# Optimization experiments

Hardware: AMD Instinct MI355X
Metric: run time of the kernel (lower is better)

Reference implementation:

```python
import jax, jax.numpy as jnp
import numpy as np

N_HEAD = 16


def setup_inputs() -> dict:
    key = jax.random.key(0)
    ks = jax.random.split(key, 3)
    B, T, C = 4, 2048, 1024
    x = jax.random.normal(ks[0], (B, T, C), dtype=jnp.float32)
    w_attn = jax.random.normal(ks[1], (3 * C, C), dtype=jnp.float32) * (1.0 / np.sqrt(C))
    b_attn = jnp.zeros((3 * C,), dtype=jnp.float32)
    w_proj = jax.random.normal(ks[2], (C, C), dtype=jnp.float32) * (1.0 / np.sqrt(C))
    b_proj = jnp.zeros((C,), dtype=jnp.float32)
    return {"x": x, "w_attn": w_attn, "b_attn": b_attn, "w_proj": w_proj, "b_proj": b_proj}


def reference(x, w_attn, b_attn, w_proj, b_proj):
    B, T, C = x.shape
    H = N_HEAD
    D = C // H
    qkv = x @ w_attn.T + b_attn                      # [B, T, 3C]
    q, k, v = jnp.split(qkv, 3, axis=-1)
    # [B, T, C] -> [B, H, T, D]
    q = q.reshape(B, T, H, D).transpose(0, 2, 1, 3)
    k = k.reshape(B, T, H, D).transpose(0, 2, 1, 3)
    v = v.reshape(B, T, H, D).transpose(0, 2, 1, 3)
    scale = 1.0 / np.sqrt(D).astype(np.float32)
    att = jnp.einsum('bhqd,bhkd->bhqk', q, k) * scale  # [B, H, T, T]
    causal = jnp.tril(jnp.ones((T, T), dtype=bool))
    att = jnp.where(causal[None, None], att, -jnp.inf)
    att = jax.nn.softmax(att, axis=-1)
    y = jnp.einsum('bhqk,bhkd->bhqd', att, v)          # [B, H, T, D]
    y = y.transpose(0, 2, 1, 3).reshape(B, T, C)
    return y @ w_proj.T + b_proj
```

## Files before the change

kernel.cpp:

```cpp
#include <hip/hip_runtime.h>
#include <hip/hip_bf16.h>
#include <stdint.h>

typedef __attribute__((ext_vector_type(8))) short bf16x8;
typedef __attribute__((ext_vector_type(4))) float f32x4;

#define MFMA16(a, b, c) __builtin_amdgcn_mfma_f32_16x16x32_bf16((a), (b), (c), 0, 0, 0)

__device__ __forceinline__ unsigned short f2bf(float f) {
  unsigned int u = __builtin_bit_cast(unsigned int, f);
  unsigned int r = (u + 0x7fffu + ((u >> 16) & 1u)) >> 16;
  return (unsigned short)r;
}

__device__ __forceinline__ void gload16(const unsigned short* g, unsigned short* lds_dst) {
  __builtin_amdgcn_global_load_lds(
      (const __attribute__((address_space(1))) unsigned int*)g,
      (__attribute__((address_space(3))) unsigned int*)lds_dst, 16, 0, 0);
}

__global__ void cvt_f32_bf16(const float* __restrict__ in, unsigned short* __restrict__ out, long n) {
  long i = ((long)blockIdx.x * blockDim.x + threadIdx.x) * 4;
  long stride = (long)gridDim.x * blockDim.x * 4;
  for (; i < n; i += stride) {
    float4 v = *(const float4*)(in + i);
    ushort4 o;
    o.x = f2bf(v.x); o.y = f2bf(v.y); o.z = f2bf(v.z); o.w = f2bf(v.w);
    *(ushort4*)(out + i) = o;
  }
}

template <int EPI>
__global__ __launch_bounds__(256, 2)
void gemm_bt(const unsigned short* __restrict__ A,
             const unsigned short* __restrict__ Bt,
             const float* __restrict__ bias,
             int M, int N, int K,
             unsigned short* __restrict__ q_out,
             unsigned short* __restrict__ k_out,
             unsigned short* __restrict__ vt_out,
             float* __restrict__ f_out) {
  alignas(16) __shared__ unsigned short Abuf[128 * 32];
  alignas(16) __shared__ unsigned short Bbuf[128 * 32];
  const int t = threadIdx.x, w = t >> 6, l = t & 63;
  const int bm = blockIdx.x, bn = blockIdx.y;
  const int wm = w >> 1, wn = w & 1;
  const int lo = l & 15, hi = l >> 4;

  f32x4 acc[4][4];
  const f32x4 zero = {0.f, 0.f, 0.f, 0.f};
#pragma unroll
  for (int i = 0; i < 4; ++i)
#pragma unroll
    for (int j = 0; j < 4; ++j) acc[i][j] = zero;

  const int srow = w * 32 + (l >> 2);
  const int scol = (l & 3) * 8;
  const long arow0 = (long)bm * 128;
  const long brow0 = (long)bn * 128;
  unsigned short* Asub = Abuf + w * 1024;
  unsigned short* Bsub = Bbuf + w * 1024;

  for (int k0 = 0; k0 < K; k0 += 32) {
    __syncthreads();
    gload16(A + (arow0 + srow) * K + k0 + scol, Asub);
    gload16(A + (arow0 + srow + 16) * K + k0 + scol, Asub + 512);
    gload16(Bt + (brow0 + srow) * K + k0 + scol, Bsub);
    gload16(Bt + (brow0 + srow + 16) * K + k0 + scol, Bsub + 512);
    __syncthreads();
    bf16x8 af[4], bfr[4];
#pragma unroll
    for (int i = 0; i < 4; ++i)
      af[i] = *(const bf16x8*)&Abuf[(wm * 64 + i * 16 + lo) * 32 + hi * 8];
#pragma unroll
    for (int j = 0; j < 4; ++j)
      bfr[j] = *(const bf16x8*)&Bbuf[(wn * 64 + j * 16 + lo) * 32 + hi * 8];
#pragma unroll
    for (int i = 0; i < 4; ++i)
#pragma unroll
      for (int j = 0; j < 4; ++j)
        acc[i][j] = MFMA16(af[i], bfr[j], acc[i][j]);
  }

#pragma unroll
  for (int i = 0; i < 4; ++i) {
#pragma unroll
    for (int j = 0; j < 4; ++j) {
#pragma unroll
      for (int r = 0; r < 4; ++r) {
        int row = bm * 128 + wm * 64 + i * 16 + hi * 4 + r;
        int col = bn * 128 + wn * 64 + j * 16 + lo;
        float v = acc[i][j][r] + bias[col];
        if (EPI == 0) {
          int b = row >> 11, tt = row & 2047;
          int seg = col >> 10, cc = col & 1023;
          int h = cc >> 6, d = cc & 63;
          long bh = (long)(b * 16 + h);
          if (seg == 0)      q_out[(bh * 2048 + tt) * 64 + d] = f2bf(v * 0.1803368801111f);
          else if (seg == 1) k_out[(bh * 2048 + tt) * 64 + d] = f2bf(v);
          else               vt_out[(bh * 64 + d) * 2048 + tt] = f2bf(v);
        } else {
          f_out[(long)row * N + col] = v;
        }
      }
    }
  }
}

__global__ __launch_bounds__(512, 4)
void attn_kernel(const unsigned short* __restrict__ Q,
                 const unsigned short* __restrict__ K,
                 const unsigned short* __restrict__ Vt,
                 unsigned short* __restrict__ Y) {
  alignas(16) __shared__ unsigned short Kbuf[2][64 * 64];
  alignas(16) __shared__ unsigned short Vbuf[2][64 * 64];
  alignas(16) __shared__ unsigned short pbuf[8][16 * 64];
  const int t = threadIdx.x, w = t >> 6, l = t & 63;
  const int lo = l & 15, hi = l >> 4;
  const int bh = blockIdx.x;
  const int p = blockIdx.y;
  const int b = bh >> 4, h = bh & 15;
  const int sA = p, sB = 15 - p;
  const int nA = 2 * p + 2;
  const int nTot = 34;
  const unsigned short* Qp = Q + (long)bh * 2048 * 64;
  const unsigned short* Kp = K + (long)bh * 2048 * 64;
  const unsigned short* Vp = Vt + (long)bh * 64 * 2048;
  unsigned short* pw = pbuf[w];

  const short one_bf = (short)0x3F80;
  const bf16x8 ones = {one_bf, one_bf, one_bf, one_bf, one_bf, one_bf, one_bf, one_bf};
  const f32x4 zero = {0.f, 0.f, 0.f, 0.f};

  const int qbA = sA * 128 + w * 16;
  const int qbB = sB * 128 + w * 16;

  bf16x8 qf0, qf1;
  float mcol;
  f32x4 lsum;
  f32x4 oacc[4];

  qf0 = *(const bf16x8*)&Qp[(qbA + lo) * 64 + hi * 8];
  qf1 = *(const bf16x8*)&Qp[(qbA + lo) * 64 + 32 + hi * 8];
  mcol = -__builtin_inff();
  lsum = zero;
#pragma unroll
  for (int dg = 0; dg < 4; ++dg) oacc[dg] = zero;

  const int srow = t >> 3;
  const int scw = ((t & 7) ^ (srow & 7)) * 8;
  const int sw = lo & 7;

#define STAGE(kvoff, bufidx)                                          \
  do {                                                                \
    unsigned short* KB_ = Kbuf[bufidx] + w * 512;                     \
    unsigned short* VB_ = Vbuf[bufidx] + w * 512;                     \
    gload16(Kp + (long)((kvoff) + srow) * 64 + scw, KB_);             \
    gload16(Vp + (long)srow * 2048 + (kvoff) + scw, VB_);             \
  } while (0)

  STAGE(0, 0);
  __syncthreads();

  for (int g = 0; g < nTot; ++g) {
    const bool inA = (g < nA);
    const int kvb = (inA ? g : g - nA) * 64;
    const int cur = g & 1;
    if (g + 1 < nTot) {
      const int jn = (g + 1 < nA) ? g + 1 : g + 1 - nA;
      STAGE(jn * 64, cur ^ 1);
    }
    const int qbase = inA ? qbA : qbB;
    if (kvb <= qbase + 15) {
      const unsigned short* KB = Kbuf[cur];
      const unsigned short* VB = Vbuf[cur];
      f32x4 s[4];
#pragma unroll
      for (int cg = 0; cg < 4; ++cg) s[cg] = zero;
      __builtin_amdgcn_s_setprio(1);
#pragma unroll
      for (int cg = 0; cg < 4; ++cg) {
        bf16x8 k0 = *(const bf16x8*)&KB[(cg * 16 + lo) * 64 + ((hi) ^ sw) * 8];
        bf16x8 k1 = *(const bf16x8*)&KB[(cg * 16 + lo) * 64 + ((4 + hi) ^ sw) * 8];
        s[cg] = MFMA16(k0, qf0, s[cg]);
        s[cg] = MFMA16(k1, qf1, s[cg]);
      }
      __builtin_amdgcn_s_setprio(0);
      if (kvb + 63 > qbase) {
        const int limit = qbase + lo - kvb;
#pragma unroll
        for (int cg = 0; cg < 4; ++cg)
#pragma unroll
          for (int r = 0; r < 4; ++r)
            if (cg * 16 + hi * 4 + r > limit) s[cg][r] = -__builtin_inff();
      }
      float pm = fmaxf(fmaxf(fmaxf(s[0][0], s[0][1]), fmaxf(s[0][2], s[0][3])),
                       fmaxf(fmaxf(s[1][0], s[1][1]), fmaxf(s[1][2], s[1][3])));
      pm = fmaxf(pm, fmaxf(fmaxf(fmaxf(s[2][0], s[2][1]), fmaxf(s[2][2], s[2][3])),
                           fmaxf(fmaxf(s[3][0], s[3][1]), fmaxf(s[3][2], s[3][3]))));
      pm = fmaxf(pm, __shfl_xor(pm, 16));
      pm = fmaxf(pm, __shfl_xor(pm, 32));
      float mn;
      if (__all(pm <= mcol + 11.54f)) {
        mn = mcol;
      } else {
        mn = fmaxf(mcol, pm);
        float a = exp2f(mcol - mn);
        mcol = mn;
        float ar[4];
#pragma unroll
        for (int r = 0; r < 4; ++r) ar[r] = __shfl(a, hi * 4 + r);
#pragma unroll
        for (int r = 0; r < 4; ++r) {
          lsum[r] *= ar[r];
#pragma unroll
          for (int dg = 0; dg < 4; ++dg) oacc[dg][r] *= ar[r];
        }
      }
#pragma unroll
      for (int cg = 0; cg < 4; ++cg) {
        float p0 = exp2f(s[cg][0] - mn);
        float p1 = exp2f(s[cg][1] - mn);
        float p2 = exp2f(s[cg][2] - mn);
        float p3 = exp2f(s[cg][3] - mn);
        unsigned int u0, u1;
        asm("v_cvt_pk_bf16_f32 %0, %1, %2" : "=v"(u0) : "v"(p0), "v"(p1));
        asm("v_cvt_pk_bf16_f32 %0, %1, %2" : "=v"(u1) : "v"(p2), "v"(p3));
        const int gg = (cg * 2 + (hi >> 1)) ^ sw;
        uint2 val; val.x = u0; val.y = u1;
        *(uint2*)&pw[lo * 64 + gg * 8 + (hi & 1) * 4] = val;
      }
      asm volatile("s_waitcnt lgkmcnt(0)" ::: "memory");
      bf16x8 pa0 = *(const bf16x8*)&pw[lo * 64 + ((hi) ^ sw) * 8];
      bf16x8 pa1 = *(const bf16x8*)&pw[lo * 64 + ((4 + hi) ^ sw) * 8];
      __builtin_amdgcn_s_setprio(1);
      lsum = MFMA16(pa0, ones, lsum);
      lsum = MFMA16(pa1, ones, lsum);
#pragma unroll
      for (int dg = 0; dg < 4; ++dg) {
        bf16x8 vv0 = *(const bf16x8*)&VB[(dg * 16 + lo) * 64 + ((hi) ^ sw) * 8];
        bf16x8 vv1 = *(const bf16x8*)&VB[(dg * 16 + lo) * 64 + ((4 + hi) ^ sw) * 8];
        oacc[dg] = MFMA16(pa0, vv0, oacc[dg]);
        oacc[dg] = MFMA16(pa1, vv1, oacc[dg]);
      }
      __builtin_amdgcn_s_setprio(0);
    }
    if (g == nA - 1) {
#pragma unroll
      for (int r = 0; r < 4; ++r) {
        float inv = 1.0f / lsum[r];
        int rowg = qbA + hi * 4 + r;
        long base = ((long)b * 2048 + rowg) * 1024 + h * 64;
#pragma unroll
        for (int dg = 0; dg < 4; ++dg)
          Y[base + dg * 16 + lo] = f2bf(oacc[dg][r] * inv);
      }
      qf0 = *(const bf16x8*)&Qp[(qbB + lo) * 64 + hi * 8];
      qf1 = *(const bf16x8*)&Qp[(qbB + lo) * 64 + 32 + hi * 8];
      mcol = -__builtin_inff();
      lsum = zero;
#pragma unroll
      for (int dg = 0; dg < 4; ++dg) oacc[dg] = zero;
    }
    __syncthreads();
  }

#pragma unroll
  for (int r = 0; r < 4; ++r) {
    float inv = 1.0f / lsum[r];
    int rowg = qbB + hi * 4 + r;
    long base = ((long)b * 2048 + rowg) * 1024 + h * 64;
#pragma unroll
    for (int dg = 0; dg < 4; ++dg)
      Y[base + dg * 16 + lo] = f2bf(oacc[dg][r] * inv);
  }
#undef STAGE
}

extern "C" void kernel_launch(void* const* d_in, const int* in_sizes, int n_in,
                              void* d_out, int out_size, void* d_ws, size_t ws_size,
                              hipStream_t stream) {
  const float* x      = (const float*)d_in[0];
  const float* w_attn = (const float*)d_in[1];
  const float* b_attn = (const float*)d_in[2];
  const float* w_proj = (const float*)d_in[3];
  const float* b_proj = (const float*)d_in[4];
  float* out = (float*)d_out;

  const long NX = 8192L * 1024;
  const long NWA = 3072L * 1024;
  const long NWP = 1024L * 1024;
  const long NQ = 64L * 2048 * 64;

  char* ws = (char*)d_ws;
  unsigned short* xb  = (unsigned short*)ws; ws += NX * 2;
  unsigned short* wab = (unsigned short*)ws; ws += NWA * 2;
  unsigned short* wpb = (unsigned short*)ws; ws += NWP * 2;
  unsigned short* qb  = (unsigned short*)ws; ws += NQ * 2;
  unsigned short* kb  = (unsigned short*)ws; ws += NQ * 2;
  unsigned short* vtb = (unsigned short*)ws; ws += NQ * 2;
  unsigned short* yb  = (unsigned short*)ws; ws += NX * 2;

  cvt_f32_bf16<<<2048, 256, 0, stream>>>(x, xb, NX);
  cvt_f32_bf16<<<768, 256, 0, stream>>>(w_attn, wab, NWA);
  cvt_f32_bf16<<<256, 256, 0, stream>>>(w_proj, wpb, NWP);

  dim3 g1(64, 24);
  gemm_bt<0><<<g1, 256, 0, stream>>>(xb, wab, b_attn, 8192, 3072, 1024,
                                     qb, kb, vtb, nullptr);
  dim3 ga(64, 8);
  attn_kernel<<<ga, 512, 0, stream>>>(qb, kb, vtb, yb);
  dim3 g2(64, 8);
  gemm_bt<1><<<g2, 256, 0, stream>>>(yb, wpb, b_proj, 8192, 1024, 1024,
                                     nullptr, nullptr, nullptr, out);
}
```

Before: 198.2 us.

## Rewrite GEMM main loop with 3-stage LDS pipeline, swizzle, and 128x256 tiles

The QKV and output-projection GEMM now uses 512-thread blocks computing 128x256 tiles with K-step 64. A triple-buffered LDS ring is fed by direct global-to-LDS loads interleaved with MFMA phases, and the LDS layout is XOR-swizzled to avoid bank conflicts. The goal is to hide global-load latency and raise MFMA utilization compared with the single-buffered loop that synced twice per 32-wide K step. It hardcodes 16 K-iterations (K=1024) and raises LDS use to about 144KB per block, which limits occupancy.

```diff
diff --git a/kernel.cpp b/kernel.cpp
--- a/kernel.cpp
+++ b/kernel.cpp
@@ -31,7 +31,7 @@
 }
 
 template <int EPI>
-__global__ __launch_bounds__(256, 2)
+__global__ __launch_bounds__(512, 2)
 void gemm_bt(const unsigned short* __restrict__ A,
              const unsigned short* __restrict__ Bt,
              const float* __restrict__ bias,
@@ -40,12 +40,12 @@
              unsigned short* __restrict__ k_out,
              unsigned short* __restrict__ vt_out,
              float* __restrict__ f_out) {
-  alignas(16) __shared__ unsigned short Abuf[128 * 32];
-  alignas(16) __shared__ unsigned short Bbuf[128 * 32];
+  alignas(16) __shared__ unsigned short Ash[3][128 * 64];
+  alignas(16) __shared__ unsigned short Bsh[3][256 * 64];
   const int t = threadIdx.x, w = t >> 6, l = t & 63;
   const int bm = blockIdx.x, bn = blockIdx.y;
-  const int wm = w >> 1, wn = w & 1;
-  const int lo = l & 15, hi = l >> 4;
+  const int wm = w >> 2, wn = w & 3;
+  const int lo = l & 15, hi = l >> 4, swk = l & 7;
 
   f32x4 acc[4][4];
   const f32x4 zero = {0.f, 0.f, 0.f, 0.f};
@@ -54,33 +54,135 @@
 #pragma unroll
     for (int j = 0; j < 4; ++j) acc[i][j] = zero;
 
-  const int srow = w * 32 + (l >> 2);
-  const int scol = (l & 3) * 8;
-  const long arow0 = (long)bm * 128;
-  const long brow0 = (long)bn * 128;
-  unsigned short* Asub = Abuf + w * 1024;
-  unsigned short* Bsub = Bbuf + w * 1024;
-
-  for (int k0 = 0; k0 < K; k0 += 32) {
-    __syncthreads();
-    gload16(A + (arow0 + srow) * K + k0 + scol, Asub);
-    gload16(A + (arow0 + srow + 16) * K + k0 + scol, Asub + 512);
-    gload16(Bt + (brow0 + srow) * K + k0 + scol, Bsub);
-    gload16(Bt + (brow0 + srow + 16) * K + k0 + scol, Bsub + 512);
-    __syncthreads();
-    bf16x8 af[4], bfr[4];
-#pragma unroll
-    for (int i = 0; i < 4; ++i)
-      af[i] = *(const bf16x8*)&Abuf[(wm * 64 + i * 16 + lo) * 32 + hi * 8];
-#pragma unroll
-    for (int j = 0; j < 4; ++j)
-      bfr[j] = *(const bf16x8*)&Bbuf[(wn * 64 + j * 16 + lo) * 32 + hi * 8];
-#pragma unroll
-    for (int i = 0; i < 4; ++i)
-#pragma unroll
-      for (int j = 0; j < 4; ++j)
-        acc[i][j] = MFMA16(af[i], bfr[j], acc[i][j]);
+  const int lr = l >> 3;
+  const int gsrc = ((l & 7) ^ lr) * 8;
+  const int rA0 = w * 16 + lr,     rA1 = w * 16 + 8 + lr;
+  const int rB0 = w * 32 + lr,     rB1 = w * 32 + 8 + lr;
+  const int rB2 = w * 32 + 16 + lr, rB3 = w * 32 + 24 + lr;
+  const unsigned short* sA0 = A + (long)(bm * 128 + rA0) * K + gsrc;
+  const unsigned short* sA1 = A + (long)(bm * 128 + rA1) * K + gsrc;
+  const unsigned short* sB0 = Bt + (long)(bn * 256 + rB0) * K + gsrc;
+  const unsigned short* sB1 = Bt + (long)(bn * 256 + rB1) * K + gsrc;
+  const unsigned short* sB2 = Bt + (long)(bn * 256 + rB2) * K + gsrc;
+  const unsigned short* sB3 = Bt + (long)(bn * 256 + rB3) * K + gsrc;
+
+#define STAGE_A(off, sb) do { unsigned short* d_ = &Ash[sb][w * 1024];        \
+    gload16(sA0 + (off), d_); gload16(sA1 + (off), d_ + 512); } while (0)
+#define STAGE_B01(off, sb) do { unsigned short* d_ = &Bsh[sb][w * 2048];      \
+    gload16(sB0 + (off), d_); gload16(sB1 + (off), d_ + 512); } while (0)
+#define STAGE_B23(off, sb) do { unsigned short* d_ = &Bsh[sb][w * 2048];      \
+    gload16(sB2 + (off), d_ + 1024); gload16(sB3 + (off), d_ + 1536); } while (0)
+
+  STAGE_A(0, 0);  STAGE_B01(0, 0);  STAGE_B23(0, 0);
+  STAGE_A(64, 1); STAGE_B01(64, 1); STAGE_B23(64, 1);
+  asm volatile("s_waitcnt vmcnt(6)" ::: "memory");
+  __builtin_amdgcn_sched_barrier(0);
+  __builtin_amdgcn_s_barrier();
+
+  const int ra = wm * 64 + lo;
+  const int rb = wn * 64 + lo;
+  const int g0 = (hi ^ swk) * 8;
+  const int g1 = ((4 + hi) ^ swk) * 8;
+
+  int cb = 0;
+  int koff = 128;
+  for (int kt = 0; kt < 16; ++kt) {
+    const unsigned short* As = Ash[cb];
+    const unsigned short* Bs = Bsh[cb];
+    int sb = cb + 2; if (sb >= 3) sb -= 3;
+    const bool st = (kt < 14);
+
+    bf16x8 a00 = *(const bf16x8*)&As[(ra)*64 + g0];
+    bf16x8 a01 = *(const bf16x8*)&As[(ra)*64 + g1];
+    bf16x8 a10 = *(const bf16x8*)&As[(ra + 16) * 64 + g0];
+    bf16x8 a11 = *(const bf16x8*)&As[(ra + 16) * 64 + g1];
+    bf16x8 b00 = *(const bf16x8*)&Bs[(rb)*64 + g0];
+    bf16x8 b01 = *(const bf16x8*)&Bs[(rb)*64 + g1];
+    bf16x8 b10 = *(const bf16x8*)&Bs[(rb + 16) * 64 + g0];
+    bf16x8 b11 = *(const bf16x8*)&Bs[(rb + 16) * 64 + g1];
+    if (st) STAGE_A(koff, sb);
+    __builtin_amdgcn_s_barrier();
+    asm volatile("s_waitcnt lgkmcnt(0)" ::: "memory");
+    __builtin_amdgcn_sched_barrier(0);
+    __builtin_amdgcn_s_setprio(1);
+    acc[0][0] = MFMA16(a00, b00, acc[0][0]);
+    acc[0][1] = MFMA16(a00, b10, acc[0][1]);
+    acc[1][0] = MFMA16(a10, b00, acc[1][0]);
+    acc[1][1] = MFMA16(a10, b10, acc[1][1]);
+    acc[0][0] = MFMA16(a01, b01, acc[0][0]);
+    acc[0][1] = MFMA16(a01, b11, acc[0][1]);
+    acc[1][0] = MFMA16(a11, b01, acc[1][0]);
+    acc[1][1] = MFMA16(a11, b11, acc[1][1]);
+    __builtin_amdgcn_s_setprio(0);
+    __builtin_amdgcn_sched_barrier(0);
+    __builtin_amdgcn_s_barrier();
+
+    bf16x8 b20 = *(const bf16x8*)&Bs[(rb + 32) * 64 + g0];
+    bf16x8 b21 = *(const bf16x8*)&Bs[(rb + 32) * 64 + g1];
+    bf16x8 b30 = *(const bf16x8*)&Bs[(rb + 48) * 64 + g0];
+    bf16x8 b31 = *(const bf16x8*)&Bs[(rb + 48) * 64 + g1];
+    if (st) STAGE_B01(koff, sb);
+    __builtin_amdgcn_s_barrier();
+    asm volatile("s_waitcnt lgkmcnt(0)" ::: "memory");
+    __builtin_amdgcn_sched_barrier(0);
+    __builtin_amdgcn_s_setprio(1);
+    acc[0][2] = MFMA16(a00, b20, acc[0][2]);
+    acc[0][3] = MFMA16(a00, b30, acc[0][3]);
+    acc[1][2] = MFMA16(a10, b20, acc[1][2]);
+    acc[1][3] = MFMA16(a10, b30, acc[1][3]);
+    acc[0][2] = MFMA16(a01, b21, acc[0][2]);
+    acc[0][3] = MFMA16(a01, b31, acc[0][3]);
+    acc[1][2] = MFMA16(a11, b21, acc[1][2]);
+    acc[1][3] = MFMA16(a11, b31, acc[1][3]);
+    __builtin_amdgcn_s_setprio(0);
+    __builtin_amdgcn_sched_barrier(0);
+    __builtin_amdgcn_s_barrier();
+
+    bf16x8 a20 = *(const bf16x8*)&As[(ra + 32) * 64 + g0];
+    bf16x8 a21 = *(const bf16x8*)&As[(ra + 32) * 64 + g1];
+    bf16x8 a30 = *(const bf16x8*)&As[(ra + 48) * 64 + g0];
+    bf16x8 a31 = *(const bf16x8*)&As[(ra + 48) * 64 + g1];
+    if (st) STAGE_B23(koff, sb);
+    __builtin_amdgcn_s_barrier();
+    asm volatile("s_waitcnt lgkmcnt(0)" ::: "memory");
+    __builtin_amdgcn_sched_barrier(0);
+    __builtin_amdgcn_s_setprio(1);
+    acc[2][2] = MFMA16(a20, b20, acc[2][2]);
+    acc[2][3] = MFMA16(a20, b30, acc[2][3]);
+    acc[3][2] = MFMA16(a30, b20, acc[3][2]);
+    acc[3][3] = MFMA16(a30, b30, acc[3][3]);
+    acc[2][2] = MFMA16(a21, b21, acc[2][2]);
+    acc[2][3] = MFMA16(a21, b31, acc[2][3]);
+    acc[3][2] = MFMA16(a31, b21, acc[3][2]);
+    acc[3][3] = MFMA16(a31, b31, acc[3][3]);
+    __builtin_amdgcn_s_setprio(0);
+    __builtin_amdgcn_sched_barrier(0);
+    __builtin_amdgcn_s_barrier();
+
+    __builtin_amdgcn_s_setprio(1);
+    acc[2][0] = MFMA16(a20, b00, acc[2][0]);
+    acc[2][1] = MFMA16(a20, b10, acc[2][1]);
+    acc[3][0] = MFMA16(a30, b00, acc[3][0]);
+    acc[3][1] = MFMA16(a30, b10, acc[3][1]);
+    acc[2][0] = MFMA16(a21, b01, acc[2][0]);
+    acc[2][1] = MFMA16(a21, b11, acc[2][1]);
+    acc[3][0] = MFMA16(a31, b01, acc[3][0]);
+    acc[3][1] = MFMA16(a31, b11, acc[3][1]);
+    __builtin_amdgcn_s_setprio(0);
+    if (kt < 14) {
+      asm volatile("s_waitcnt vmcnt(6)" ::: "memory");
+    } else if (kt == 14) {
+      asm volatile("s_waitcnt vmcnt(0)" ::: "memory");
+    }
+    __builtin_amdgcn_sched_barrier(0);
+    __builtin_amdgcn_s_barrier();
+
+    cb += 1; if (cb == 3) cb = 0;
+    koff += 64;
   }
+#undef STAGE_A
+#undef STAGE_B01
+#undef STAGE_B23
 
 #pragma unroll
   for (int i = 0; i < 4; ++i) {
@@ -89,7 +191,7 @@
 #pragma unroll
       for (int r = 0; r < 4; ++r) {
         int row = bm * 128 + wm * 64 + i * 16 + hi * 4 + r;
-        int col = bn * 128 + wn * 64 + j * 16 + lo;
+        int col = bn * 256 + wn * 64 + j * 16 + lo;
         float v = acc[i][j][r] + bias[col];
         if (EPI == 0) {
           int b = row >> 11, tt = row & 2047;
@@ -305,12 +407,12 @@
   cvt_f32_bf16<<<768, 256, 0, stream>>>(w_attn, wab, NWA);
   cvt_f32_bf16<<<256, 256, 0, stream>>>(w_proj, wpb, NWP);
 
-  dim3 g1(64, 24);
-  gemm_bt<0><<<g1, 256, 0, stream>>>(xb, wab, b_attn, 8192, 3072, 1024,
+  dim3 g1(64, 12);
+  gemm_bt<0><<<g1, 512, 0, stream>>>(xb, wab, b_attn, 8192, 3072, 1024,
                                      qb, kb, vtb, nullptr);
   dim3 ga(64, 8);
   attn_kernel<<<ga, 512, 0, stream>>>(qb, kb, vtb, yb);
-  dim3 g2(64, 8);
-  gemm_bt<1><<<g2, 256, 0, stream>>>(yb, wpb, b_proj, 8192, 1024, 1024,
+  dim3 g2(64, 4);
+  gemm_bt<1><<<g2, 512, 0, stream>>>(yb, wpb, b_proj, 8192, 1024, 1024,
                                      nullptr, nullptr, nullptr, out);
 }
```

New measurement: 195.3 us. About the same (-1.4%).

## Rewrite GEMM as 256x256 tile, 8-wave, double-buffered pipelined kernel with swizzled LDS

Applied to the files above, without the earlier changes.

The GEMM kernel moves from a 128x128 tile with 4 waves and single-buffered K=32 steps to a 256x256 tile with 8 waves. It uses K=64 steps with double-buffered LDS split into halves, an XOR swizzle on the LDS column layout, and an interleaved schedule. That schedule issues the next tile's global-to-LDS loads between MFMA quadrants, using explicit waitcnt, barriers and setprio. The aim is to hide global-load latency behind MFMA work, cut bank conflicts, and raise data reuse per block. The cost is larger register (acc[8][4]) and LDS footprint, fewer blocks (grid shrinks to 32x12 and 32x4), and a hardcoded K loop count of 16 that assumes K=1024.

```diff
diff --git a/kernel.cpp b/kernel.cpp
--- a/kernel.cpp
+++ b/kernel.cpp
@@ -31,7 +31,7 @@
 }
 
 template <int EPI>
-__global__ __launch_bounds__(256, 2)
+__global__ __launch_bounds__(512, 2)
 void gemm_bt(const unsigned short* __restrict__ A,
              const unsigned short* __restrict__ Bt,
              const float* __restrict__ bias,
@@ -40,56 +40,156 @@
              unsigned short* __restrict__ k_out,
              unsigned short* __restrict__ vt_out,
              float* __restrict__ f_out) {
-  alignas(16) __shared__ unsigned short Abuf[128 * 32];
-  alignas(16) __shared__ unsigned short Bbuf[128 * 32];
+  alignas(16) __shared__ unsigned short Alds[2][2][128 * 64];
+  alignas(16) __shared__ unsigned short Blds[2][2][128 * 64];
   const int t = threadIdx.x, w = t >> 6, l = t & 63;
   const int bm = blockIdx.x, bn = blockIdx.y;
-  const int wm = w >> 1, wn = w & 1;
-  const int lo = l & 15, hi = l >> 4;
-
-  f32x4 acc[4][4];
+  const int wm = w >> 2, wn = w & 3;
+  const int lo = l & 15, hi = l >> 4, swk = lo & 7;
+
+  f32x4 acc[8][4];
   const f32x4 zero = {0.f, 0.f, 0.f, 0.f};
 #pragma unroll
-  for (int i = 0; i < 4; ++i)
+  for (int i = 0; i < 8; ++i)
 #pragma unroll
     for (int j = 0; j < 4; ++j) acc[i][j] = zero;
 
-  const int srow = w * 32 + (l >> 2);
-  const int scol = (l & 3) * 8;
-  const long arow0 = (long)bm * 128;
-  const long brow0 = (long)bn * 128;
-  unsigned short* Asub = Abuf + w * 1024;
-  unsigned short* Bsub = Bbuf + w * 1024;
-
-  for (int k0 = 0; k0 < K; k0 += 32) {
-    __syncthreads();
-    gload16(A + (arow0 + srow) * K + k0 + scol, Asub);
-    gload16(A + (arow0 + srow + 16) * K + k0 + scol, Asub + 512);
-    gload16(Bt + (brow0 + srow) * K + k0 + scol, Bsub);
-    gload16(Bt + (brow0 + srow + 16) * K + k0 + scol, Bsub + 512);
-    __syncthreads();
-    bf16x8 af[4], bfr[4];
-#pragma unroll
-    for (int i = 0; i < 4; ++i)
-      af[i] = *(const bf16x8*)&Abuf[(wm * 64 + i * 16 + lo) * 32 + hi * 8];
-#pragma unroll
-    for (int j = 0; j < 4; ++j)
-      bfr[j] = *(const bf16x8*)&Bbuf[(wn * 64 + j * 16 + lo) * 32 + hi * 8];
-#pragma unroll
-    for (int i = 0; i < 4; ++i)
-#pragma unroll
-      for (int j = 0; j < 4; ++j)
-        acc[i][j] = MFMA16(af[i], bfr[j], acc[i][j]);
+  const int sr = t >> 3;
+  const int gsrcE = ((t & 7) ^ (sr & 7)) * 8;
+  const unsigned short* Asrc = A + (long)(bm * 256 + sr) * K + gsrcE;
+  const unsigned short* Bsrc = Bt + (long)(bn * 256 + ((sr >> 5) << 6) + (sr & 31)) * K + gsrcE;
+
+#define STAGE_AH(sb, qh, koff) do {                                    \
+    unsigned short* d_ = &Alds[sb][qh][w * 512];                       \
+    const unsigned short* s_ = Asrc + (long)(qh) * 64 * K + (koff);    \
+    gload16(s_, d_); gload16(s_ + 128L * K, d_ + 4096); } while (0)
+#define STAGE_BH(sb, hh, koff) do {                                    \
+    unsigned short* d_ = &Blds[sb][hh][w * 512];                       \
+    const unsigned short* s_ = Bsrc + (long)(hh) * 32 * K + (koff);    \
+    gload16(s_, d_); gload16(s_ + 128L * K, d_ + 4096); } while (0)
+
+  STAGE_AH(0, 0, 0);
+  STAGE_BH(0, 0, 0);
+  STAGE_BH(0, 1, 0);
+  STAGE_AH(0, 1, 0);
+  asm volatile("s_waitcnt vmcnt(4)" ::: "memory");
+  __builtin_amdgcn_sched_barrier(0);
+  __builtin_amdgcn_s_barrier();
+
+  const int lrA = (wm * 64 + lo) * 64;
+  const int lrB = (wn * 32 + lo) * 64;
+  const int gk0 = ((hi) ^ swk) * 8;
+  const int gk1 = ((4 + hi) ^ swk) * 8;
+
+  bf16x8 af[4][2], blo[2][2], bhi[2][2];
+
+  for (int kt = 0; kt < 16; ++kt) {
+    const int c = kt & 1, nb = c ^ 1;
+    const bool st = (kt < 15);
+    const int koff = (kt + 1) * 64;
+    const unsigned short* A0 = Alds[c][0];
+    const unsigned short* A1 = Alds[c][1];
+    const unsigned short* B0 = Blds[c][0];
+    const unsigned short* B1 = Blds[c][1];
+
+#pragma unroll
+    for (int ii = 0; ii < 4; ++ii) {
+      af[ii][0] = *(const bf16x8*)&A0[lrA + ii * 1024 + gk0];
+      af[ii][1] = *(const bf16x8*)&A0[lrA + ii * 1024 + gk1];
+    }
+#pragma unroll
+    for (int jj = 0; jj < 2; ++jj) {
+      blo[jj][0] = *(const bf16x8*)&B0[lrB + jj * 1024 + gk0];
+      blo[jj][1] = *(const bf16x8*)&B0[lrB + jj * 1024 + gk1];
+    }
+    if (st) STAGE_AH(nb, 0, koff);
+    __builtin_amdgcn_s_barrier();
+    asm volatile("s_waitcnt lgkmcnt(0)" ::: "memory");
+    __builtin_amdgcn_sched_barrier(0);
+    __builtin_amdgcn_s_setprio(1);
+#pragma unroll
+    for (int ii = 0; ii < 4; ++ii)
+#pragma unroll
+      for (int jj = 0; jj < 2; ++jj) {
+        acc[ii][jj] = MFMA16(af[ii][0], blo[jj][0], acc[ii][jj]);
+        acc[ii][jj] = MFMA16(af[ii][1], blo[jj][1], acc[ii][jj]);
+      }
+    __builtin_amdgcn_s_setprio(0);
+    if (st) { asm volatile("s_waitcnt vmcnt(4)" ::: "memory"); }
+    else    { asm volatile("s_waitcnt vmcnt(2)" ::: "memory"); }
+    __builtin_amdgcn_sched_barrier(0);
+    __builtin_amdgcn_s_barrier();
+
+#pragma unroll
+    for (int jj = 0; jj < 2; ++jj) {
+      bhi[jj][0] = *(const bf16x8*)&B1[lrB + jj * 1024 + gk0];
+      bhi[jj][1] = *(const bf16x8*)&B1[lrB + jj * 1024 + gk1];
+    }
+    if (st) STAGE_BH(nb, 0, koff);
+    __builtin_amdgcn_s_barrier();
+    asm volatile("s_waitcnt lgkmcnt(0)" ::: "memory");
+    __builtin_amdgcn_sched_barrier(0);
+    __builtin_amdgcn_s_setprio(1);
+#pragma unroll
+    for (int ii = 0; ii < 4; ++ii)
+#pragma unroll
+      for (int jj = 0; jj < 2; ++jj) {
+        acc[ii][2 + jj] = MFMA16(af[ii][0], bhi[jj][0], acc[ii][2 + jj]);
+        acc[ii][2 + jj] = MFMA16(af[ii][1], bhi[jj][1], acc[ii][2 + jj]);
+      }
+    __builtin_amdgcn_s_setprio(0);
+    if (st) { asm volatile("s_waitcnt vmcnt(4)" ::: "memory"); }
+    else    { asm volatile("s_waitcnt vmcnt(0)" ::: "memory"); }
+    __builtin_amdgcn_sched_barrier(0);
+    __builtin_amdgcn_s_barrier();
+
+#pragma unroll
+    for (int ii = 0; ii < 4; ++ii) {
+      af[ii][0] = *(const bf16x8*)&A1[lrA + ii * 1024 + gk0];
+      af[ii][1] = *(const bf16x8*)&A1[lrA + ii * 1024 + gk1];
+    }
+    if (st) STAGE_BH(nb, 1, koff);
+    __builtin_amdgcn_s_barrier();
+    asm volatile("s_waitcnt lgkmcnt(0)" ::: "memory");
+    __builtin_amdgcn_sched_barrier(0);
+    __builtin_amdgcn_s_setprio(1);
+#pragma unroll
+    for (int ii = 0; ii < 4; ++ii)
+#pragma unroll
+      for (int jj = 0; jj < 2; ++jj) {
+        acc[4 + ii][2 + jj] = MFMA16(af[ii][0], bhi[jj][0], acc[4 + ii][2 + jj]);
+        acc[4 + ii][2 + jj] = MFMA16(af[ii][1], bhi[jj][1], acc[4 + ii][2 + jj]);
+      }
+    __builtin_amdgcn_s_setprio(0);
+    asm volatile("s_waitcnt vmcnt(4)" ::: "memory");
+    __builtin_amdgcn_sched_barrier(0);
+    __builtin_amdgcn_s_barrier();
+
+    if (st) STAGE_AH(nb, 1, koff);
+    __builtin_amdgcn_s_setprio(1);
+#pragma unroll
+    for (int ii = 0; ii < 4; ++ii)
+#pragma unroll
+      for (int jj = 0; jj < 2; ++jj) {
+        acc[4 + ii][jj] = MFMA16(af[ii][0], blo[jj][0], acc[4 + ii][jj]);
+        acc[4 + ii][jj] = MFMA16(af[ii][1], blo[jj][1], acc[4 + ii][jj]);
+      }
+    __builtin_amdgcn_s_setprio(0);
+    asm volatile("s_waitcnt vmcnt(4)" ::: "memory");
+    __builtin_amdgcn_sched_barrier(0);
+    __builtin_amdgcn_s_barrier();
   }
-
-#pragma unroll
-  for (int i = 0; i < 4; ++i) {
+#undef STAGE_AH
+#undef STAGE_BH
+
+#pragma unroll
+  for (int i = 0; i < 8; ++i) {
 #pragma unroll
     for (int j = 0; j < 4; ++j) {
 #pragma unroll
       for (int r = 0; r < 4; ++r) {
-        int row = bm * 128 + wm * 64 + i * 16 + hi * 4 + r;
-        int col = bn * 128 + wn * 64 + j * 16 + lo;
+        int row = bm * 256 + wm * 128 + i * 16 + hi * 4 + r;
+        int col = bn * 256 + wn * 64 + j * 16 + lo;
         float v = acc[i][j][r] + bias[col];
         if (EPI == 0) {
           int b = row >> 11, tt = row & 2047;
@@ -305,12 +405,12 @@
   cvt_f32_bf16<<<768, 256, 0, stream>>>(w_attn, wab, NWA);
   cvt_f32_bf16<<<256, 256, 0, stream>>>(w_proj, wpb, NWP);
 
-  dim3 g1(64, 24);
-  gemm_bt<0><<<g1, 256, 0, stream>>>(xb, wab, b_attn, 8192, 3072, 1024,
+  dim3 g1(32, 12);
+  gemm_bt<0><<<g1, 512, 0, stream>>>(xb, wab, b_attn, 8192, 3072, 1024,
                                      qb, kb, vtb, nullptr);
   dim3 ga(64, 8);
   attn_kernel<<<ga, 512, 0, stream>>>(qb, kb, vtb, yb);
-  dim3 g2(64, 8);
-  gemm_bt<1><<<g2, 256, 0, stream>>>(yb, wpb, b_proj, 8192, 1024, 1024,
+  dim3 g2(32, 4);
+  gemm_bt<1><<<g2, 512, 0, stream>>>(yb, wpb, b_proj, 8192, 1024, 1024,
                                      nullptr, nullptr, nullptr, out);
 }
```

Result: slower. 208.6 us (+5.3%).
